# Kernel optimization log

Hardware: AMD Instinct MI355X
Metric: run time of the kernel (lower is better)

## Reference

```python
import jax, jax.numpy as jnp
import numpy as np

EPS = 1e-8
PAD = 1  # kernel // 2 for kernel=3


def setup_inputs() -> dict:
    key = jax.random.key(0)
    k1, k2, k3, k4, k5 = jax.random.split(key, 5)
    b, c, h, w = 16, 256, 64, 64
    out_ch, kernel, style_dim = 256, 3, 512
    x = jax.random.normal(k1, (b, c, h, w), dtype=jnp.float32)
    style = jax.random.normal(k2, (b, style_dim), dtype=jnp.float32)
    # learned params
    weight = jax.random.normal(k3, (1, out_ch, c, kernel, kernel), dtype=jnp.float32)
    lim = 1.0 / np.sqrt(style_dim)
    mod_w = jax.random.uniform(k4, (c, style_dim), minval=-lim, maxval=lim, dtype=jnp.float32)
    mod_b = jax.random.uniform(k5, (c,), minval=-lim, maxval=lim, dtype=jnp.float32)
    return {"x": x, "style": style, "weight": weight, "mod_w": mod_w, "mod_b": mod_b}


def reference(x, style, weight, mod_w, mod_b):
    # s[b,i]: per-sample, per-input-channel modulation from the style Linear
    s = style @ mod_w.T + mod_b                     # [b, in_ch]
    w = weight[0]                                    # [out_ch, in_ch, k, k]
    # demod factor: sum_{i,kh,kw} (w[o,i,kh,kw]*s[b,i])^2 = sum_i s^2 * sum_kk w^2
    w_sq = jnp.sum(w * w, axis=(2, 3))               # [out_ch, in_ch]
    d = jax.lax.rsqrt(jnp.einsum('oi,bi->bo', w_sq, s * s) + EPS)  # [b, out_ch]
    # modulate input channels instead of materializing per-sample weights
    xs = x * s[:, :, None, None]                     # [b, in_ch, h, w]
    y = jax.lax.conv_general_dilated(
        xs, w, window_strides=(1, 1), padding=[(PAD, PAD), (PAD, PAD)],
        dimension_numbers=('NCHW', 'OIHW', 'NCHW'))
    return y * d[:, :, None, None]                   # [b, out_ch, h, w]
```

## Files before the change

kernel.cpp:

```cpp
#include <hip/hip_runtime.h>
#include <hip/hip_bf16.h>
#include <cstdint>
#include <cstddef>

typedef __bf16 bf16_t;
typedef __bf16 bf16x4 __attribute__((ext_vector_type(4)));
typedef __bf16 bf16x8 __attribute__((ext_vector_type(8)));
typedef float  f32x4  __attribute__((ext_vector_type(4)));

#define NB   16
#define NC   256
#define NO   256
#define SD   512
#define NPIX 4096
#define CPAD 36

#define WS_S   0
#define WS_WSQ 32768
#define WS_WT  294912

__global__ __launch_bounds__(256) void prep1(
    const float* __restrict__ style, const float* __restrict__ weight,
    const float* __restrict__ mod_w, const float* __restrict__ mod_b,
    float* __restrict__ s_buf, float* __restrict__ wsq, bf16_t* __restrict__ wT)
{
    const int blk = blockIdx.x;
    const int tid = threadIdx.x;
    if (blk < 16) {
        const int b = blk, i = tid;
        const float* st = style + b * SD;
        const float* mw = mod_w + i * SD;
        float acc = 0.f;
        for (int k = 0; k < SD; k += 4) {
            float4 a = *(const float4*)(st + k);
            float4 c = *(const float4*)(mw + k);
            acc += a.x * c.x + a.y * c.y + a.z * c.z + a.w * c.w;
        }
        s_buf[b * NC + i] = acc + mod_b[i];
    } else {
        const int o = blk - 16, i = tid;
        const float* wp = weight + (o * NC + i) * 9;
        float q = 0.f;
        #pragma unroll
        for (int t = 0; t < 9; ++t) {
            float v = wp[t];
            q += v * v;
            wT[t * (NO * NC) + o * NC + i] = (bf16_t)v;
        }
        wsq[o * NC + i] = q;
    }
}

__device__ __forceinline__ void stage_a(const bf16_t* __restrict__ wT_tap,
                                        int o0, int ic0, bf16_t* dst, int tid)
{
    #pragma unroll
    for (int it = 0; it < 2; ++it) {
        int s = it * 256 + tid;
        const bf16_t* g = wT_tap + (o0 + (s & 127)) * NC + ic0 + (s >> 7) * 8;
        __builtin_amdgcn_global_load_lds(
            (const __attribute__((address_space(1))) void*)g,
            (__attribute__((address_space(3))) void*)(dst + s * 8),
            16, 0, 0);
    }
}

__global__ __launch_bounds__(256, 2) void conv_mfma(
    const float* __restrict__ x,
    const bf16_t* __restrict__ wT,
    const float* __restrict__ s_buf,
    const float* __restrict__ wsq,
    float* __restrict__ out)
{
    __shared__ bf16_t lds_a[4][4096];
    __shared__ bf16_t lds_b[4 * 64 * CPAD];

    const int tid   = threadIdx.x;
    const int lane  = tid & 63;
    const int wv    = tid >> 6;
    const int wo    = wv >> 1;
    const int wp    = wv & 1;
    const int pt    = blockIdx.x;
    const int o0    = blockIdx.y * 128;
    const int batch = blockIdx.z;
    const int row0  = pt * 2;

    const int l15 = lane & 15;
    const int kg  = lane >> 4;
    const int k0  = kg * 8;

    const int colB = tid & 63;
    const int cgrp = tid >> 6;

    f32x4 acc[4][4];
    #pragma unroll
    for (int i = 0; i < 4; ++i)
        #pragma unroll
        for (int j = 0; j < 4; ++j) {
            f32x4 z = {0.f, 0.f, 0.f, 0.f};
            acc[i][j] = z;
        }

    bf16x8 bzero;
    #pragma unroll
    for (int j = 0; j < 8; ++j) bzero[j] = (bf16_t)0.f;

    const size_t TSTR = (size_t)NO * NC;
    bf16_t* lds_a0 = &lds_a[0][0];

    float vx[4][8];
    float sv[8];
    auto XLOAD = [&](int ic0) {
        const float* sp = s_buf + batch * NC + ic0 + cgrp * 8;
        float4 sa = *(const float4*)sp;
        float4 sb = *(const float4*)(sp + 4);
        sv[0]=sa.x; sv[1]=sa.y; sv[2]=sa.z; sv[3]=sa.w;
        sv[4]=sb.x; sv[5]=sb.y; sv[6]=sb.z; sv[7]=sb.w;
        const float* xbase = x + (size_t)(batch * NC + ic0 + cgrp * 8) * NPIX + colB;
        #pragma unroll
        for (int r = 0; r < 4; ++r) {
            const int gy = row0 - 1 + r;
            const bool valid = ((unsigned)gy < 64u);
            const float* rp = xbase + gy * 64;
            #pragma unroll
            for (int j = 0; j < 8; ++j)
                vx[r][j] = valid ? rp[j * NPIX] : 0.f;
        }
    };
    auto BWRITE = [&]() {
        #pragma unroll
        for (int r = 0; r < 4; ++r) {
            const int lbase = (r * 64 + colB) * CPAD + cgrp * 8;
            #pragma unroll
            for (int half = 0; half < 2; ++half) {
                union { bf16_t h[4]; uint2 u; } pk;
                #pragma unroll
                for (int j = 0; j < 4; ++j)
                    pk.h[j] = (bf16_t)(vx[r][half * 4 + j] * sv[half * 4 + j]);
                *(uint2*)&lds_b[lbase + half * 4] = pk.u;
            }
        }
    };

    XLOAD(0);
    BWRITE();
    stage_a(wT,        o0, 0, lds_a0 + 0 * 4096, tid);
    stage_a(wT + TSTR, o0, 0, lds_a0 + 1 * 4096, tid);
    asm volatile("s_waitcnt lgkmcnt(0)" ::: "memory");
    __builtin_amdgcn_sched_barrier(0);
    __builtin_amdgcn_s_barrier();

    #pragma unroll 1
    for (int chunk = 0; chunk < 8; ++chunk) {
        const int ic0 = chunk * 32;

        #pragma unroll
        for (int tap = 0; tap < 9; ++tap) {
            bf16_t* nbuf = lds_a0 + (size_t)((chunk + tap + 2) & 3) * 4096;
            if (tap < 7) {
                stage_a(wT + (size_t)(tap + 2) * TSTR, o0, ic0, nbuf, tid);
                asm volatile("s_waitcnt vmcnt(4)" ::: "memory");
            } else if (chunk < 7) {
                stage_a(wT + (size_t)(tap - 7) * TSTR, o0, ic0 + 32, nbuf, tid);
                asm volatile("s_waitcnt vmcnt(4)" ::: "memory");
            } else if (tap == 7) {
                asm volatile("s_waitcnt vmcnt(2)" ::: "memory");
            } else {
                asm volatile("s_waitcnt vmcnt(0)" ::: "memory");
            }
            __builtin_amdgcn_sched_barrier(0);
            __builtin_amdgcn_s_barrier();

            const bf16_t* abuf = lds_a0 + (size_t)((chunk + tap) & 3) * 4096;
            const int kh = tap / 3, kw = tap % 3;

            bf16x8 af[4];
            #pragma unroll
            for (int of = 0; of < 4; ++of)
                af[of] = *(const bf16x8*)&abuf[kg * 1024 + (wo * 64 + of * 16 + l15) * 8];

            const int r = wp + kh;
            bf16x8 bfr[4];
            #pragma unroll
            for (int nf = 0; nf < 4; ++nf) {
                const int c = nf * 16 + l15 + kw - 1;
                if ((unsigned)c < 64u) {
                    const bf16_t* p = &lds_b[(r * 64 + c) * CPAD + k0];
                    bf16x4 lo = *(const bf16x4*)p;
                    bf16x4 hi = *(const bf16x4*)(p + 4);
                    bfr[nf] = __builtin_shufflevector(lo, hi, 0, 1, 2, 3, 4, 5, 6, 7);
                } else {
                    bfr[nf] = bzero;
                }
            }

            #pragma unroll
            for (int of = 0; of < 4; ++of)
                #pragma unroll
                for (int nf = 0; nf < 4; ++nf)
                    acc[of][nf] = __builtin_amdgcn_mfma_f32_16x16x32_bf16(
                        af[of], bfr[nf], acc[of][nf], 0, 0, 0);
        }

        if (chunk < 7) {
            XLOAD(ic0 + 32);
            __builtin_amdgcn_sched_barrier(0);
            __builtin_amdgcn_s_barrier();
            BWRITE();
            asm volatile("s_waitcnt lgkmcnt(0)" ::: "memory");
            __builtin_amdgcn_sched_barrier(0);
            __builtin_amdgcn_s_barrier();
        }
    }

    __syncthreads();
    float* d_sh = (float*)&lds_b[0];
    {
        const int ol   = tid >> 1;
        const int half = tid & 1;
        const float* wq = wsq + (size_t)(o0 + ol) * NC + half * 128;
        const float* sb = s_buf + batch * NC + half * 128;
        float sum = 0.f;
        #pragma unroll 4
        for (int i = 0; i < 128; i += 4) {
            float4 w4 = *(const float4*)(wq + i);
            float4 s4 = *(const float4*)(sb + i);
            sum += w4.x * s4.x * s4.x + w4.y * s4.y * s4.y
                 + w4.z * s4.z * s4.z + w4.w * s4.w * s4.w;
        }
        sum += __shfl_xor(sum, 1);
        if (half == 0) d_sh[ol] = rsqrtf(sum + 1e-8f);
    }
    __syncthreads();

    const int p_base = pt * 128 + wp * 64;
    #pragma unroll
    for (int of = 0; of < 4; ++of) {
        #pragma unroll
        for (int rg = 0; rg < 4; ++rg) {
            const int o_l = wo * 64 + of * 16 + (lane >> 4) * 4 + rg;
            const float dv = d_sh[o_l];
            const size_t obase = (size_t)(batch * NO + o0 + o_l) * NPIX;
            #pragma unroll
            for (int nf = 0; nf < 4; ++nf) {
                const int p_g = p_base + nf * 16 + l15;
                out[obase + p_g] = acc[of][nf][rg] * dv;
            }
        }
    }
}

extern "C" void kernel_launch(void* const* d_in, const int* in_sizes, int n_in,
                              void* d_out, int out_size, void* d_ws, size_t ws_size,
                              hipStream_t stream)
{
    const float* x      = (const float*)d_in[0];
    const float* style  = (const float*)d_in[1];
    const float* weight = (const float*)d_in[2];
    const float* mod_w  = (const float*)d_in[3];
    const float* mod_b  = (const float*)d_in[4];
    float* out = (float*)d_out;

    char* ws = (char*)d_ws;
    float*  s_buf = (float*)(ws + WS_S);
    float*  wsq   = (float*)(ws + WS_WSQ);
    bf16_t* wT    = (bf16_t*)(ws + WS_WT);

    hipLaunchKernelGGL(prep1, dim3(272), dim3(256), 0, stream,
                       style, weight, mod_w, mod_b, s_buf, wsq, wT);
    hipLaunchKernelGGL(conv_mfma, dim3(32, 2, 16), dim3(256), 0, stream,
                       x, wT, s_buf, wsq, out);
}
```

Before: 235.1 us.

## Stage weight taps in groups of three with double-buffered LDS superstages

Weight tiles are now loaded three taps (one kernel row) at a time into two alternating LDS superbuffers, replacing the per-tap four-buffer ring. This cuts block barriers from nine per input-channel chunk to about three. The next chunk's activation load is issued earlier so it overlaps the last row's MFMAs, and wave priority is raised around the MFMA section. The cost is more LDS per block (six weight tiles instead of four), which could limit occupancy. Each wave waits only on its own loads before reading a superbuffer that other waves also filled, so there is a possible cross-wave race on weight data.

```diff
diff --git a/kernel.cpp b/kernel.cpp
--- a/kernel.cpp
+++ b/kernel.cpp
@@ -51,17 +51,22 @@
     }
 }
 
-__device__ __forceinline__ void stage_a(const bf16_t* __restrict__ wT_tap,
-                                        int o0, int ic0, bf16_t* dst, int tid)
-{
-    #pragma unroll
-    for (int it = 0; it < 2; ++it) {
-        int s = it * 256 + tid;
-        const bf16_t* g = wT_tap + (o0 + (s & 127)) * NC + ic0 + (s >> 7) * 8;
-        __builtin_amdgcn_global_load_lds(
-            (const __attribute__((address_space(1))) void*)g,
-            (__attribute__((address_space(3))) void*)(dst + s * 8),
-            16, 0, 0);
+__device__ __forceinline__ void stage_a3(const bf16_t* __restrict__ wT_base,
+                                         int tap0, int o0, int ic0,
+                                         bf16_t* dst, int tid)
+{
+    #pragma unroll
+    for (int t = 0; t < 3; ++t) {
+        const bf16_t* wt = wT_base + (size_t)(tap0 + t) * (NO * NC);
+        #pragma unroll
+        for (int it = 0; it < 2; ++it) {
+            int s = it * 256 + tid;
+            const bf16_t* g = wt + (o0 + (s & 127)) * NC + ic0 + (s >> 7) * 8;
+            __builtin_amdgcn_global_load_lds(
+                (const __attribute__((address_space(1))) void*)g,
+                (__attribute__((address_space(3))) void*)(dst + t * 4096 + s * 8),
+                16, 0, 0);
+        }
     }
 }
 
@@ -72,7 +77,7 @@
     const float* __restrict__ wsq,
     float* __restrict__ out)
 {
-    __shared__ bf16_t lds_a[4][4096];
+    __shared__ bf16_t lds_a[6][4096];
     __shared__ bf16_t lds_b[4 * 64 * CPAD];
 
     const int tid   = threadIdx.x;
@@ -105,8 +110,8 @@
     #pragma unroll
     for (int j = 0; j < 8; ++j) bzero[j] = (bf16_t)0.f;
 
-    const size_t TSTR = (size_t)NO * NC;
     bf16_t* lds_a0 = &lds_a[0][0];
+    #define SUPER(idx) (lds_a0 + (size_t)((idx) & 1) * (3 * 4096))
 
     float vx[4][8];
     float sv[8];
@@ -142,69 +147,72 @@
         }
     };
 
+    stage_a3(wT, 0, o0, 0, SUPER(0), tid);
     XLOAD(0);
     BWRITE();
-    stage_a(wT,        o0, 0, lds_a0 + 0 * 4096, tid);
-    stage_a(wT + TSTR, o0, 0, lds_a0 + 1 * 4096, tid);
-    asm volatile("s_waitcnt lgkmcnt(0)" ::: "memory");
-    __builtin_amdgcn_sched_barrier(0);
-    __builtin_amdgcn_s_barrier();
+    __syncthreads();
 
     #pragma unroll 1
-    for (int chunk = 0; chunk < 8; ++chunk) {
-        const int ic0 = chunk * 32;
-
-        #pragma unroll
-        for (int tap = 0; tap < 9; ++tap) {
-            bf16_t* nbuf = lds_a0 + (size_t)((chunk + tap + 2) & 3) * 4096;
-            if (tap < 7) {
-                stage_a(wT + (size_t)(tap + 2) * TSTR, o0, ic0, nbuf, tid);
-                asm volatile("s_waitcnt vmcnt(4)" ::: "memory");
-            } else if (chunk < 7) {
-                stage_a(wT + (size_t)(tap - 7) * TSTR, o0, ic0 + 32, nbuf, tid);
-                asm volatile("s_waitcnt vmcnt(4)" ::: "memory");
-            } else if (tap == 7) {
-                asm volatile("s_waitcnt vmcnt(2)" ::: "memory");
+    for (int ch = 0; ch < 8; ++ch) {
+        const int ic0 = ch * 32;
+
+        #pragma unroll
+        for (int i = 0; i < 3; ++i) {
+            bf16_t* cur = SUPER(ch + i);
+            bf16_t* nxt = SUPER(ch + i + 1);
+
+            if (i < 2) {
+                stage_a3(wT, 3 * (i + 1), o0, ic0, nxt, tid);
+                asm volatile("s_waitcnt vmcnt(6)" ::: "memory");
+            } else if (ch < 7) {
+                stage_a3(wT, 0, o0, ic0 + 32, nxt, tid);
+                asm volatile("s_waitcnt vmcnt(6)" ::: "memory");
             } else {
                 asm volatile("s_waitcnt vmcnt(0)" ::: "memory");
             }
             __builtin_amdgcn_sched_barrier(0);
-            __builtin_amdgcn_s_barrier();
-
-            const bf16_t* abuf = lds_a0 + (size_t)((chunk + tap) & 3) * 4096;
-            const int kh = tap / 3, kw = tap % 3;
-
-            bf16x8 af[4];
-            #pragma unroll
-            for (int of = 0; of < 4; ++of)
-                af[of] = *(const bf16x8*)&abuf[kg * 1024 + (wo * 64 + of * 16 + l15) * 8];
-
-            const int r = wp + kh;
-            bf16x8 bfr[4];
-            #pragma unroll
-            for (int nf = 0; nf < 4; ++nf) {
-                const int c = nf * 16 + l15 + kw - 1;
-                if ((unsigned)c < 64u) {
-                    const bf16_t* p = &lds_b[(r * 64 + c) * CPAD + k0];
-                    bf16x4 lo = *(const bf16x4*)p;
-                    bf16x4 hi = *(const bf16x4*)(p + 4);
-                    bfr[nf] = __builtin_shufflevector(lo, hi, 0, 1, 2, 3, 4, 5, 6, 7);
-                } else {
-                    bfr[nf] = bzero;
+
+            if (i == 2 && ch < 7)
+                XLOAD(ic0 + 32);
+
+            const int r = wp + i;
+            __builtin_amdgcn_s_setprio(1);
+            #pragma unroll
+            for (int t = 0; t < 3; ++t) {
+                const bf16_t* abuf = cur + t * 4096;
+                bf16x8 af[4];
+                #pragma unroll
+                for (int of = 0; of < 4; ++of)
+                    af[of] = *(const bf16x8*)&abuf[kg * 1024 + (wo * 64 + of * 16 + l15) * 8];
+
+                bf16x8 bfr[4];
+                #pragma unroll
+                for (int nf = 0; nf < 4; ++nf) {
+                    const int c = nf * 16 + l15 + t - 1;
+                    if ((unsigned)c < 64u) {
+                        const bf16_t* p = &lds_b[(r * 64 + c) * CPAD + k0];
+                        bf16x4 lo = *(const bf16x4*)p;
+                        bf16x4 hi = *(const bf16x4*)(p + 4);
+                        bfr[nf] = __builtin_shufflevector(lo, hi, 0, 1, 2, 3, 4, 5, 6, 7);
+                    } else {
+                        bfr[nf] = bzero;
+                    }
                 }
-            }
-
-            #pragma unroll
-            for (int of = 0; of < 4; ++of)
-                #pragma unroll
-                for (int nf = 0; nf < 4; ++nf)
-                    acc[of][nf] = __builtin_amdgcn_mfma_f32_16x16x32_bf16(
-                        af[of], bfr[nf], acc[of][nf], 0, 0, 0);
-        }
-
-        if (chunk < 7) {
-            XLOAD(ic0 + 32);
-            __builtin_amdgcn_sched_barrier(0);
+
+                #pragma unroll
+                for (int of = 0; of < 4; ++of)
+                    #pragma unroll
+                    for (int nf = 0; nf < 4; ++nf)
+                        acc[of][nf] = __builtin_amdgcn_mfma_f32_16x16x32_bf16(
+                            af[of], bfr[nf], acc[of][nf], 0, 0, 0);
+            }
+            __builtin_amdgcn_s_setprio(0);
+
+            if (i < 2)
+                __builtin_amdgcn_s_barrier();
+        }
+
+        if (ch < 7) {
             __builtin_amdgcn_s_barrier();
             BWRITE();
             asm volatile("s_waitcnt lgkmcnt(0)" ::: "memory");
@@ -212,6 +220,7 @@
             __builtin_amdgcn_s_barrier();
         }
     }
+    #undef SUPER
 
     __syncthreads();
     float* d_sh = (float*)&lds_b[0];
```

New measurement: 243.1 us. 3.4% more time.
